# Kernel optimization log

Hardware: AMD Instinct MI355X
Metric: run time of the kernel (lower is better)

The kernel has to match this reference:

```python
import jax, jax.numpy as jnp
import numpy as np

EPS = 1e-5


def setup_inputs() -> dict:
    key = jax.random.key(0)
    k1, k2, k3, k4, k5 = jax.random.split(key, 5)
    B, C, F, O = 32, 64, 16384, 128
    x = jax.random.normal(k1, (B, C, F), dtype=jnp.float32)
    adj = jax.random.randint(k2, (B, F, 4), 0, F, dtype=jnp.int64)
    # Conv1d(C, O, kernel_size=2, stride=2): weight [O, C, 2], bias [O]
    W = jax.random.normal(k3, (O, C, 2), dtype=jnp.float32) * (1.0 / np.sqrt(2 * C))
    b = jax.random.normal(k4, (O,), dtype=jnp.float32) * 0.01
    gamma = jnp.ones((O,), dtype=jnp.float32)
    beta_bn = jnp.zeros((O,), dtype=jnp.float32)
    return {"x": x, "adj": adj, "W": W, "b": b, "gamma": gamma, "beta_bn": beta_bn}


def reference(x, adj, W, b, gamma, beta_bn):
    B, C, F = x.shape
    xt = jnp.transpose(x, (0, 2, 1))                      # [B, F, C]
    # per-batch neighbor gather: re[b, f, k, :] = xt[b, adj[b, f, k], :]
    re = xt[jnp.arange(B)[:, None, None], adj]            # [B, F, 4, C]
    target = re[:, :, 0]                                  # [B, F, C] (alpha)
    neighbors = re[:, :, 1:]                              # [B, F, 3, C]
    beta_f = jnp.sum(jnp.abs(target[:, :, None, :] - neighbors), axis=2)  # [B, F, C]
    # Conv1d(k=2, s=2) over interleaved (alpha, beta) pairs == two matmuls
    y = (jnp.einsum("bfc,oc->bof", target, W[:, :, 0])
         + jnp.einsum("bfc,oc->bof", beta_f, W[:, :, 1])
         + b[None, :, None])                              # [B, O, F]
    # BatchNorm1d (training-mode batch stats over batch and length dims)
    mean = jnp.mean(y, axis=(0, 2), keepdims=True)
    var = jnp.var(y, axis=(0, 2), keepdims=True)
    y = (y - mean) * jax.lax.rsqrt(var + EPS)
    y = y * gamma[None, :, None] + beta_bn[None, :, None]
    return jax.nn.relu(y)
```

## Files before the change

kernel.cpp:

```cpp
#include <hip/hip_runtime.h>

#define B_DIM 32
#define C_DIM 64
#define F_DIM 16384
#define O_DIM 128
#define NBLK ((F_DIM / 64) * B_DIM)

typedef __attribute__((ext_vector_type(8))) short short8;
typedef __attribute__((ext_vector_type(4))) float f32x4;

__device__ __forceinline__ ushort f2bf(float f) {
    union { float f; uint u; } v; v.f = f;
    return (ushort)((v.u + 0x7FFFu + ((v.u >> 16) & 1u)) >> 16);
}
__device__ __forceinline__ float bflo(uint u) {
    union { uint u; float f; } v; v.u = u << 16; return v.f;
}
__device__ __forceinline__ float bfhi(uint u) {
    union { uint u; float f; } v; v.u = u & 0xFFFF0000u; return v.f;
}

__global__ __launch_bounds__(256) void k_transpose(const float* __restrict__ x,
                                                   ushort* __restrict__ xt,
                                                   const float* __restrict__ W,
                                                   ushort* __restrict__ Wtg) {
    __shared__ float tile[64][65];
    const int b  = blockIdx.y;
    const int f0 = blockIdx.x * 64;
    const int t  = threadIdx.x;
    const int fl = t & 63;
    const int q  = t >> 6;

    const float* xb = x + (size_t)b * C_DIM * F_DIM;
    #pragma unroll
    for (int i = 0; i < 16; ++i) {
        const int c = q + i * 4;
        tile[c][fl] = __builtin_nontemporal_load(&xb[(size_t)c * F_DIM + f0 + fl]);
    }

    if (blockIdx.x == 0 && blockIdx.y == 0 && t < 128) {
        const int o = t;
        #pragma unroll 8
        for (int c = 0; c < C_DIM; ++c) {
            Wtg[o * 128 + c]      = f2bf(W[o * 128 + c * 2]);
            Wtg[o * 128 + 64 + c] = f2bf(W[o * 128 + c * 2 + 1]);
        }
    }

    __syncthreads();

    const int f  = t >> 2;
    const int ch = t & 3;
    union { ushort s[16]; uint4 v[2]; } u;
    #pragma unroll
    for (int j = 0; j < 16; ++j)
        u.s[j] = f2bf(tile[ch * 16 + j][f]);
    ushort* dst = xt + ((size_t)b * F_DIM + f0 + f) * C_DIM + ch * 16;
    *(uint4*)(dst)     = u.v[0];
    *(uint4*)(dst + 8) = u.v[1];
}

template <int MODE>
__global__ __launch_bounds__(256, 3) void k_compute_t(const ushort* __restrict__ xt,
                                                      const int*    __restrict__ adj,
                                                      const ushort* __restrict__ Wtg,
                                                      const float*  __restrict__ bias,
                                                      const float*  __restrict__ ss,
                                                      float*        __restrict__ y,
                                                      float*        __restrict__ part) {
    __shared__ __align__(16) char Asm[64 * 256];
    __shared__ __align__(16) char Wsm[128 * 256];

    const int bid = blockIdx.x;
    const int tg  = (bid & 7) * (NBLK / 8) + (bid >> 3);
    const int b   = tg >> 8;
    const int f0  = (tg & 255) * 64;
    const int t   = threadIdx.x;

    const int p  = t >> 2;
    const int ch = t & 3;
    const int4 a4 = ((const int4*)adj)[(size_t)b * F_DIM + f0 + p];
    const char* xb = (const char*)(xt + (size_t)b * F_DIM * C_DIM);
    const char* r0 = xb + (size_t)a4.x * 128 + ch * 32;
    const char* r1 = xb + (size_t)a4.y * 128 + ch * 32;
    const char* r2 = xb + (size_t)a4.z * 128 + ch * 32;
    const char* r3 = xb + (size_t)a4.w * 128 + ch * 32;
    uint4 g[8];
    g[0] = *(const uint4*)(r0);  g[1] = *(const uint4*)(r0 + 16);
    g[2] = *(const uint4*)(r1);  g[3] = *(const uint4*)(r1 + 16);
    g[4] = *(const uint4*)(r2);  g[5] = *(const uint4*)(r2 + 16);
    g[6] = *(const uint4*)(r3);  g[7] = *(const uint4*)(r3 + 16);

    {
        const uint4* src = (const uint4*)Wtg;
        #pragma unroll
        for (int jj = 0; jj < 8; ++jj) {
            const int fb    = t * 128 + jj * 16;
            const int o     = fb >> 8;
            const int inner = fb & 255;
            *(uint4*)(Wsm + (o << 8) + (inner ^ ((o & 7) << 4))) = src[fb >> 4];
        }
    }

    {
        const int sw = (p & 7) << 4;
        char* Arow = Asm + p * 256;
        #pragma unroll
        for (int h = 0; h < 2; ++h) {
            const uint4 t0 = g[h], n1 = g[2 + h], n2 = g[4 + h], n3 = g[6 + h];
            *(uint4*)(Arow + ((ch * 32 + h * 16) ^ sw)) = t0;
            const uint tu[4] = { t0.x, t0.y, t0.z, t0.w };
            const uint au[4] = { n1.x, n1.y, n1.z, n1.w };
            const uint bu[4] = { n2.x, n2.y, n2.z, n2.w };
            const uint cu[4] = { n3.x, n3.y, n3.z, n3.w };
            uint bt[4];
            #pragma unroll
            for (int qq = 0; qq < 4; ++qq) {
                const float tl = bflo(tu[qq]), th = bfhi(tu[qq]);
                const float lo = fabsf(tl - bflo(au[qq])) + fabsf(tl - bflo(bu[qq])) + fabsf(tl - bflo(cu[qq]));
                const float hi = fabsf(th - bfhi(au[qq])) + fabsf(th - bfhi(bu[qq])) + fabsf(th - bfhi(cu[qq]));
                bt[qq] = (uint)f2bf(lo) | ((uint)f2bf(hi) << 16);
            }
            *(uint4*)(Arow + ((128 + ch * 32 + h * 16) ^ sw)) =
                make_uint4(bt[0], bt[1], bt[2], bt[3]);
        }
    }

    __syncthreads();

    const int w     = t >> 6;
    const int l     = t & 63;
    const int col16 = l & 15;
    const int gg    = l >> 4;
    const int swl   = (l & 7) << 4;

    f32x4 acc[8];
    #pragma unroll
    for (int s = 0; s < 8; ++s) {
        const float bv = bias[s * 16 + col16];
        acc[s] = (f32x4){ bv, bv, bv, bv };
    }

    const char* ArowR = Asm + (w * 16 + col16) * 256;
    #pragma unroll
    for (int kk = 0; kk < 4; ++kk) {
        const int koff = kk * 64 + gg * 16;
        const short8 af = *(const short8*)(ArowR + (koff ^ swl));
        #pragma unroll
        for (int s = 0; s < 8; ++s) {
            const short8 bf = *(const short8*)(Wsm + (s * 16 + col16) * 256 + (koff ^ swl));
            acc[s] = __builtin_amdgcn_mfma_f32_16x16x32_bf16(af, bf, acc[s], 0, 0, 0);
        }
    }

    if (MODE == 0) {
        __shared__ float sm_s[4][128];
        __shared__ float sm_q[4][128];
        #pragma unroll
        for (int s = 0; s < 8; ++s) {
            float ps = acc[s].x + acc[s].y + acc[s].z + acc[s].w;
            float pq = acc[s].x * acc[s].x + acc[s].y * acc[s].y
                     + acc[s].z * acc[s].z + acc[s].w * acc[s].w;
            ps += __shfl_xor(ps, 16, 64);  pq += __shfl_xor(pq, 16, 64);
            ps += __shfl_xor(ps, 32, 64);  pq += __shfl_xor(pq, 32, 64);
            if (gg == 0) {
                sm_s[w][s * 16 + col16] = ps;
                sm_q[w][s * 16 + col16] = pq;
            }
        }
        __syncthreads();
        if (t < 128) {
            const float a = sm_s[0][t] + sm_s[1][t] + sm_s[2][t] + sm_s[3][t];
            const float c = sm_q[0][t] + sm_q[1][t] + sm_q[2][t] + sm_q[3][t];
            part[(size_t)t * NBLK + bid]         = a;
            part[(size_t)(128 + t) * NBLK + bid] = c;
        }
    } else {
        const int fbase = f0 + w * 16 + gg * 4;
        #pragma unroll
        for (int s = 0; s < 8; ++s) {
            const int o = s * 16 + col16;
            const float sc = ss[o];
            const float sh = ss[O_DIM + o];
            f32x4 v = acc[s];
            v.x = fmaxf(fmaf(v.x, sc, sh), 0.f);
            v.y = fmaxf(fmaf(v.y, sc, sh), 0.f);
            v.z = fmaxf(fmaf(v.z, sc, sh), 0.f);
            v.w = fmaxf(fmaf(v.w, sc, sh), 0.f);
            __builtin_nontemporal_store(v, (f32x4*)(y + ((size_t)b * O_DIM + o) * F_DIM + fbase));
        }
    }
}

__global__ __launch_bounds__(256) void k_reduce_finalize(const float* __restrict__ part,
                                                         const float* __restrict__ gamma,
                                                         const float* __restrict__ beta_bn,
                                                         float* __restrict__ ss) {
    const int o = blockIdx.x;
    const int t = threadIdx.x;
    const float4* p1 = (const float4*)(part + (size_t)o * NBLK);
    const float4* p2 = (const float4*)(part + (size_t)(128 + o) * NBLK);
    float s = 0.f, q = 0.f;
    for (int i = t; i < NBLK / 4; i += 256) {
        const float4 v = p1[i];
        s += v.x + v.y + v.z + v.w;
        const float4 u = p2[i];
        q += u.x + u.y + u.z + u.w;
    }
    #pragma unroll
    for (int off = 32; off > 0; off >>= 1) {
        s += __shfl_down(s, off, 64);
        q += __shfl_down(q, off, 64);
    }
    __shared__ float ls[8];
    const int wid = t >> 6, lane = t & 63;
    if (lane == 0) { ls[wid] = s; ls[4 + wid] = q; }
    __syncthreads();
    if (t == 0) {
        const float ts = ls[0] + ls[1] + ls[2] + ls[3];
        const float tq = ls[4] + ls[5] + ls[6] + ls[7];
        const float n    = (float)B_DIM * (float)F_DIM;
        const float mean = ts / n;
        const float var  = tq / n - mean * mean;
        const float sc   = gamma[o] * rsqrtf(var + 1e-5f);
        ss[o]         = sc;
        ss[O_DIM + o] = beta_bn[o] - mean * sc;
    }
}

__global__ __launch_bounds__(256) void k_compute_slow(const float* __restrict__ xsrc,
                                                      const int*   __restrict__ adj,
                                                      const float* __restrict__ W,
                                                      const float* __restrict__ bias,
                                                      float*       __restrict__ y) {
    const int b = blockIdx.y;
    const int f = blockIdx.x * 256 + threadIdx.x;
    const int4 a = ((const int4*)adj)[(size_t)b * F_DIM + f];
    float tg[64], bt[64];
    const float* base = xsrc + (size_t)b * C_DIM * F_DIM;
    #pragma unroll
    for (int c = 0; c < 64; ++c) {
        const float tv = base[(size_t)c * F_DIM + a.x];
        const float n1 = base[(size_t)c * F_DIM + a.y];
        const float n2 = base[(size_t)c * F_DIM + a.z];
        const float n3 = base[(size_t)c * F_DIM + a.w];
        tg[c] = tv;
        bt[c] = fabsf(tv - n1) + fabsf(tv - n2) + fabsf(tv - n3);
    }
    float* yb = y + (size_t)b * O_DIM * F_DIM + f;
    const float2* W2 = (const float2*)W;
    #pragma unroll 4
    for (int o = 0; o < O_DIM; ++o) {
        float acc = bias[o];
        #pragma unroll
        for (int c = 0; c < 64; ++c) {
            const float2 wv = W2[o * 64 + c];
            acc = fmaf(tg[c], wv.x, fmaf(bt[c], wv.y, acc));
        }
        yb[(size_t)o * F_DIM] = acc;
    }
}

__global__ __launch_bounds__(256) void k_stats(const float* __restrict__ y,
                                               float* __restrict__ stats) {
    const int o = blockIdx.x;
    const int b = blockIdx.y;
    const float4* row = (const float4*)(y + ((size_t)b * O_DIM + o) * F_DIM);
    float s = 0.f, s2 = 0.f;
    for (int i = threadIdx.x; i < F_DIM / 4; i += 256) {
        const float4 v = row[i];
        s  += v.x + v.y + v.z + v.w;
        s2 += v.x * v.x + v.y * v.y + v.z * v.z + v.w * v.w;
    }
    #pragma unroll
    for (int off = 32; off > 0; off >>= 1) {
        s  += __shfl_down(s,  off, 64);
        s2 += __shfl_down(s2, off, 64);
    }
    __shared__ float ls[4], ls2[4];
    const int wid = threadIdx.x >> 6, lane = threadIdx.x & 63;
    if (lane == 0) { ls[wid] = s; ls2[wid] = s2; }
    __syncthreads();
    if (threadIdx.x == 0) {
        atomicAdd(&stats[o],         ls[0] + ls[1] + ls[2] + ls[3]);
        atomicAdd(&stats[O_DIM + o], ls2[0] + ls2[1] + ls2[2] + ls2[3]);
    }
}

__global__ void k_finalize(const float* __restrict__ stats,
                           const float* __restrict__ gamma,
                           const float* __restrict__ beta_bn,
                           float* __restrict__ ss) {
    const int o = threadIdx.x;
    if (o < O_DIM) {
        const float n    = (float)B_DIM * (float)F_DIM;
        const float mean = stats[o] / n;
        const float var  = stats[O_DIM + o] / n - mean * mean;
        const float sc   = gamma[o] * rsqrtf(var + 1e-5f);
        ss[o]         = sc;
        ss[O_DIM + o] = beta_bn[o] - mean * sc;
    }
}

__global__ __launch_bounds__(256) void k_norm(float* __restrict__ y,
                                              const float* __restrict__ ss) {
    const size_t n4 = (size_t)B_DIM * O_DIM * F_DIM / 4;
    const size_t stride = (size_t)gridDim.x * blockDim.x;
    float4* y4 = (float4*)y;
    for (size_t i = (size_t)blockIdx.x * blockDim.x + threadIdx.x; i < n4; i += stride) {
        const int o = (int)((i >> 12) & (O_DIM - 1));
        const float sc = ss[o];
        const float sh = ss[O_DIM + o];
        float4 v = y4[i];
        v.x = fmaxf(fmaf(v.x, sc, sh), 0.f);
        v.y = fmaxf(fmaf(v.y, sc, sh), 0.f);
        v.z = fmaxf(fmaf(v.z, sc, sh), 0.f);
        v.w = fmaxf(fmaf(v.w, sc, sh), 0.f);
        y4[i] = v;
    }
}

extern "C" void kernel_launch(void* const* d_in, const int* in_sizes, int n_in,
                              void* d_out, int out_size, void* d_ws, size_t ws_size,
                              hipStream_t stream) {
    const float* x       = (const float*)d_in[0];
    const int*   adj     = (const int*)  d_in[1];
    const float* W       = (const float*)d_in[2];
    const float* bias    = (const float*)d_in[3];
    const float* gamma   = (const float*)d_in[4];
    const float* beta_bn = (const float*)d_in[5];
    float* out = (float*)d_out;

    const size_t XT_B   = (size_t)B_DIM * F_DIM * C_DIM * 2;
    const size_t PART_B = (size_t)2 * O_DIM * NBLK * sizeof(float);

    float*  stats = (float*)d_ws;
    float*  ss    = (float*)((char*)d_ws + 1024);
    ushort* Wtg   = (ushort*)((char*)d_ws + 4096);
    ushort* xt    = (ushort*)((char*)d_ws + 65536);
    float*  part  = (float*)((char*)d_ws + 65536 + XT_B);

    const size_t need = 65536 + XT_B + PART_B;

    if (ws_size >= need) {
        k_transpose<<<dim3(F_DIM / 64, B_DIM), 256, 0, stream>>>(x, xt, W, Wtg);
        k_compute_t<0><<<dim3(NBLK), 256, 0, stream>>>(xt, adj, Wtg, bias, nullptr, nullptr, part);
        k_reduce_finalize<<<O_DIM, 256, 0, stream>>>(part, gamma, beta_bn, ss);
        k_compute_t<1><<<dim3(NBLK), 256, 0, stream>>>(xt, adj, Wtg, bias, ss, out, nullptr);
    } else {
        hipMemsetAsync(stats, 0, 2 * O_DIM * sizeof(float), stream);
        k_compute_slow<<<dim3(F_DIM / 256, B_DIM), 256, 0, stream>>>(x, adj, W, bias, out);
        k_stats<<<dim3(O_DIM, B_DIM), 256, 0, stream>>>(out, stats);
        k_finalize<<<1, 128, 0, stream>>>(stats, gamma, beta_bn, ss);
        k_norm<<<2048, 256, 0, stream>>>(out, ss);
    }
}
```

Baseline: 196.5 us.

## Build MFMA A-fragments directly in registers, dropping the LDS A staging tile

Each lane now gathers exactly the channels it needs for its MFMA A-operand fragments and computes the beta (abs-diff sum) values in registers. This removes the 16KB shared A tile, its swizzled writes and reads, and it reorders the K loop so each output slice runs four MFMAs back to back. The smaller LDS footprint lets the launch bound rise to 4 blocks per CU. In exchange, the gathers use 16B accesses at 64B stride per row instead of contiguous 32B chunks, and register pressure may rise under the tighter occupancy bound.

```diff
diff --git a/kernel.cpp b/kernel.cpp
--- a/kernel.cpp
+++ b/kernel.cpp
@@ -18,6 +18,15 @@
 }
 __device__ __forceinline__ float bfhi(uint u) {
     union { uint u; float f; } v; v.u = u & 0xFFFF0000u; return v.f;
+}
+__device__ __forceinline__ uint beta_pair(uint tu, uint au, uint bu, uint cu) {
+    const float tl = bflo(tu), th = bfhi(tu);
+    const float lo = fabsf(tl - bflo(au)) + fabsf(tl - bflo(bu)) + fabsf(tl - bflo(cu));
+    const float hi = fabsf(th - bfhi(au)) + fabsf(th - bfhi(bu)) + fabsf(th - bfhi(cu));
+    return (uint)f2bf(lo) | ((uint)f2bf(hi) << 16);
+}
+__device__ __forceinline__ short8 as_s8(uint4 u) {
+    union { uint4 u; short8 s; } cv; cv.u = u; return cv.s;
 }
 
 __global__ __launch_bounds__(256) void k_transpose(const float* __restrict__ x,
@@ -61,14 +70,13 @@
 }
 
 template <int MODE>
-__global__ __launch_bounds__(256, 3) void k_compute_t(const ushort* __restrict__ xt,
+__global__ __launch_bounds__(256, 4) void k_compute_t(const ushort* __restrict__ xt,
                                                       const int*    __restrict__ adj,
                                                       const ushort* __restrict__ Wtg,
                                                       const float*  __restrict__ bias,
                                                       const float*  __restrict__ ss,
                                                       float*        __restrict__ y,
                                                       float*        __restrict__ part) {
-    __shared__ __align__(16) char Asm[64 * 256];
     __shared__ __align__(16) char Wsm[128 * 256];
 
     const int bid = blockIdx.x;
@@ -77,19 +85,27 @@
     const int f0  = (tg & 255) * 64;
     const int t   = threadIdx.x;
 
-    const int p  = t >> 2;
-    const int ch = t & 3;
+    const int w     = t >> 6;
+    const int l     = t & 63;
+    const int col16 = l & 15;
+    const int g     = l >> 4;
+    const int co    = g * 16;
+    const int p     = w * 16 + col16;
+
     const int4 a4 = ((const int4*)adj)[(size_t)b * F_DIM + f0 + p];
     const char* xb = (const char*)(xt + (size_t)b * F_DIM * C_DIM);
-    const char* r0 = xb + (size_t)a4.x * 128 + ch * 32;
-    const char* r1 = xb + (size_t)a4.y * 128 + ch * 32;
-    const char* r2 = xb + (size_t)a4.z * 128 + ch * 32;
-    const char* r3 = xb + (size_t)a4.w * 128 + ch * 32;
-    uint4 g[8];
-    g[0] = *(const uint4*)(r0);  g[1] = *(const uint4*)(r0 + 16);
-    g[2] = *(const uint4*)(r1);  g[3] = *(const uint4*)(r1 + 16);
-    g[4] = *(const uint4*)(r2);  g[5] = *(const uint4*)(r2 + 16);
-    g[6] = *(const uint4*)(r3);  g[7] = *(const uint4*)(r3 + 16);
+    const char* r0 = xb + (size_t)a4.x * 128 + co;
+    const char* r1 = xb + (size_t)a4.y * 128 + co;
+    const char* r2 = xb + (size_t)a4.z * 128 + co;
+    const char* r3 = xb + (size_t)a4.w * 128 + co;
+    uint4 g0 = *(const uint4*)(r0);
+    uint4 g1 = *(const uint4*)(r0 + 64);
+    uint4 g2 = *(const uint4*)(r1);
+    uint4 g3 = *(const uint4*)(r1 + 64);
+    uint4 g4 = *(const uint4*)(r2);
+    uint4 g5 = *(const uint4*)(r2 + 64);
+    uint4 g6 = *(const uint4*)(r3);
+    uint4 g7 = *(const uint4*)(r3 + 64);
 
     {
         const uint4* src = (const uint4*)Wtg;
@@ -101,38 +117,18 @@
             *(uint4*)(Wsm + (o << 8) + (inner ^ ((o & 7) << 4))) = src[fb >> 4];
         }
     }
-
-    {
-        const int sw = (p & 7) << 4;
-        char* Arow = Asm + p * 256;
-        #pragma unroll
-        for (int h = 0; h < 2; ++h) {
-            const uint4 t0 = g[h], n1 = g[2 + h], n2 = g[4 + h], n3 = g[6 + h];
-            *(uint4*)(Arow + ((ch * 32 + h * 16) ^ sw)) = t0;
-            const uint tu[4] = { t0.x, t0.y, t0.z, t0.w };
-            const uint au[4] = { n1.x, n1.y, n1.z, n1.w };
-            const uint bu[4] = { n2.x, n2.y, n2.z, n2.w };
-            const uint cu[4] = { n3.x, n3.y, n3.z, n3.w };
-            uint bt[4];
-            #pragma unroll
-            for (int qq = 0; qq < 4; ++qq) {
-                const float tl = bflo(tu[qq]), th = bfhi(tu[qq]);
-                const float lo = fabsf(tl - bflo(au[qq])) + fabsf(tl - bflo(bu[qq])) + fabsf(tl - bflo(cu[qq]));
-                const float hi = fabsf(th - bfhi(au[qq])) + fabsf(th - bfhi(bu[qq])) + fabsf(th - bfhi(cu[qq]));
-                bt[qq] = (uint)f2bf(lo) | ((uint)f2bf(hi) << 16);
-            }
-            *(uint4*)(Arow + ((128 + ch * 32 + h * 16) ^ sw)) =
-                make_uint4(bt[0], bt[1], bt[2], bt[3]);
-        }
-    }
-
     __syncthreads();
 
-    const int w     = t >> 6;
-    const int l     = t & 63;
-    const int col16 = l & 15;
-    const int gg    = l >> 4;
-    const int swl   = (l & 7) << 4;
+    short8 af0 = as_s8(g0);
+    short8 af1 = as_s8(g1);
+    short8 af2 = as_s8(make_uint4(beta_pair(g0.x, g2.x, g4.x, g6.x),
+                                  beta_pair(g0.y, g2.y, g4.y, g6.y),
+                                  beta_pair(g0.z, g2.z, g4.z, g6.z),
+                                  beta_pair(g0.w, g2.w, g4.w, g6.w)));
+    short8 af3 = as_s8(make_uint4(beta_pair(g1.x, g3.x, g5.x, g7.x),
+                                  beta_pair(g1.y, g3.y, g5.y, g7.y),
+                                  beta_pair(g1.z, g3.z, g5.z, g7.z),
+                                  beta_pair(g1.w, g3.w, g5.w, g7.w)));
 
     f32x4 acc[8];
     #pragma unroll
@@ -141,16 +137,18 @@
         acc[s] = (f32x4){ bv, bv, bv, bv };
     }
 
-    const char* ArowR = Asm + (w * 16 + col16) * 256;
-    #pragma unroll
-    for (int kk = 0; kk < 4; ++kk) {
-        const int koff = kk * 64 + gg * 16;
-        const short8 af = *(const short8*)(ArowR + (koff ^ swl));
-        #pragma unroll
-        for (int s = 0; s < 8; ++s) {
-            const short8 bf = *(const short8*)(Wsm + (s * 16 + col16) * 256 + (koff ^ swl));
-            acc[s] = __builtin_amdgcn_mfma_f32_16x16x32_bf16(af, bf, acc[s], 0, 0, 0);
-        }
+    const int swl = (col16 & 7) << 4;
+    #pragma unroll
+    for (int s = 0; s < 8; ++s) {
+        const char* Wrow = Wsm + (s * 16 + col16) * 256;
+        acc[s] = __builtin_amdgcn_mfma_f32_16x16x32_bf16(
+                     af0, *(const short8*)(Wrow + ((0 * 64 + g * 16) ^ swl)), acc[s], 0, 0, 0);
+        acc[s] = __builtin_amdgcn_mfma_f32_16x16x32_bf16(
+                     af1, *(const short8*)(Wrow + ((1 * 64 + g * 16) ^ swl)), acc[s], 0, 0, 0);
+        acc[s] = __builtin_amdgcn_mfma_f32_16x16x32_bf16(
+                     af2, *(const short8*)(Wrow + ((2 * 64 + g * 16) ^ swl)), acc[s], 0, 0, 0);
+        acc[s] = __builtin_amdgcn_mfma_f32_16x16x32_bf16(
+                     af3, *(const short8*)(Wrow + ((3 * 64 + g * 16) ^ swl)), acc[s], 0, 0, 0);
     }
 
     if (MODE == 0) {
@@ -163,7 +161,7 @@
                      + acc[s].z * acc[s].z + acc[s].w * acc[s].w;
             ps += __shfl_xor(ps, 16, 64);  pq += __shfl_xor(pq, 16, 64);
             ps += __shfl_xor(ps, 32, 64);  pq += __shfl_xor(pq, 32, 64);
-            if (gg == 0) {
+            if (g == 0) {
                 sm_s[w][s * 16 + col16] = ps;
                 sm_q[w][s * 16 + col16] = pq;
             }
@@ -176,7 +174,7 @@
             part[(size_t)(128 + t) * NBLK + bid] = c;
         }
     } else {
-        const int fbase = f0 + w * 16 + gg * 4;
+        const int fbase = f0 + w * 16 + g * 4;
         #pragma unroll
         for (int s = 0; s < 8; ++s) {
             const int o = s * 16 + col16;
```

Measured after the change: 208.7 us. 6.2% more time.

## Process eight tiles per block with prefetched gathers overlapping MFMA work

Applied to the files above, without the earlier changes.

Each compute block now handles eight consecutive 64-row tiles instead of one. The W tile load into shared memory and the bias/scale reads are amortized across tiles, and the gather loads for the next tile are issued before the MFMA and epilogue of the current one. Per-block statistics accumulate in registers across the tiles, which shrinks the partial-sum buffer and the work of the reduce kernel. The cost is more register pressure, two barriers per tile, and an eighth as many blocks, which lowers parallelism on the grid.

```diff
diff --git a/kernel.cpp b/kernel.cpp
--- a/kernel.cpp
+++ b/kernel.cpp
@@ -4,7 +4,9 @@
 #define C_DIM 64
 #define F_DIM 16384
 #define O_DIM 128
-#define NBLK ((F_DIM / 64) * B_DIM)
+#define NBLK  ((F_DIM / 64) * B_DIM)
+#define TPB   8
+#define NBLK3 (NBLK / TPB)
 
 typedef __attribute__((ext_vector_type(8))) short short8;
 typedef __attribute__((ext_vector_type(4))) float f32x4;
@@ -18,6 +20,12 @@
 }
 __device__ __forceinline__ float bfhi(uint u) {
     union { uint u; float f; } v; v.u = u & 0xFFFF0000u; return v.f;
+}
+__device__ __forceinline__ uint beta_pair(uint tu, uint au, uint bu, uint cu) {
+    const float tl = bflo(tu), th = bfhi(tu);
+    const float lo = fabsf(tl - bflo(au)) + fabsf(tl - bflo(bu)) + fabsf(tl - bflo(cu));
+    const float hi = fabsf(th - bfhi(au)) + fabsf(th - bfhi(bu)) + fabsf(th - bfhi(cu));
+    return (uint)f2bf(lo) | ((uint)f2bf(hi) << 16);
 }
 
 __global__ __launch_bounds__(256) void k_transpose(const float* __restrict__ x,
@@ -71,25 +79,40 @@
     __shared__ __align__(16) char Asm[64 * 256];
     __shared__ __align__(16) char Wsm[128 * 256];
 
-    const int bid = blockIdx.x;
-    const int tg  = (bid & 7) * (NBLK / 8) + (bid >> 3);
-    const int b   = tg >> 8;
-    const int f0  = (tg & 255) * 64;
-    const int t   = threadIdx.x;
+    const int bid  = blockIdx.x;
+    const int tg0  = ((bid & 7) * (NBLK3 / 8) + (bid >> 3)) * TPB;
+    const int b    = tg0 >> 8;
+    const int tloc = tg0 & 255;
+    const int t    = threadIdx.x;
 
     const int p  = t >> 2;
     const int ch = t & 3;
-    const int4 a4 = ((const int4*)adj)[(size_t)b * F_DIM + f0 + p];
-    const char* xb = (const char*)(xt + (size_t)b * F_DIM * C_DIM);
-    const char* r0 = xb + (size_t)a4.x * 128 + ch * 32;
-    const char* r1 = xb + (size_t)a4.y * 128 + ch * 32;
-    const char* r2 = xb + (size_t)a4.z * 128 + ch * 32;
-    const char* r3 = xb + (size_t)a4.w * 128 + ch * 32;
-    uint4 g[8];
-    g[0] = *(const uint4*)(r0);  g[1] = *(const uint4*)(r0 + 16);
-    g[2] = *(const uint4*)(r1);  g[3] = *(const uint4*)(r1 + 16);
-    g[4] = *(const uint4*)(r2);  g[5] = *(const uint4*)(r2 + 16);
-    g[6] = *(const uint4*)(r3);  g[7] = *(const uint4*)(r3 + 16);
+    const int4* adjp = (const int4*)adj + (size_t)b * F_DIM;
+    const char* xb   = (const char*)(xt + (size_t)b * F_DIM * C_DIM);
+
+    const int4 a0 = adjp[(tloc + 0) * 64 + p];
+    const int4 a1 = adjp[(tloc + 1) * 64 + p];
+    const int4 a2 = adjp[(tloc + 2) * 64 + p];
+    const int4 a3 = adjp[(tloc + 3) * 64 + p];
+    const int4 a4_ = adjp[(tloc + 4) * 64 + p];
+    const int4 a5 = adjp[(tloc + 5) * 64 + p];
+    const int4 a6 = adjp[(tloc + 6) * 64 + p];
+    const int4 a7 = adjp[(tloc + 7) * 64 + p];
+
+    uint4 g0, g1, g2, g3, g4, g5, g6, g7;
+    #define ISSUE(a)                                                          \
+        do {                                                                  \
+            g0 = *(const uint4*)(xb + (size_t)(a).x * 128 + ch * 32);         \
+            g1 = *(const uint4*)(xb + (size_t)(a).x * 128 + ch * 32 + 16);    \
+            g2 = *(const uint4*)(xb + (size_t)(a).y * 128 + ch * 32);         \
+            g3 = *(const uint4*)(xb + (size_t)(a).y * 128 + ch * 32 + 16);    \
+            g4 = *(const uint4*)(xb + (size_t)(a).z * 128 + ch * 32);         \
+            g5 = *(const uint4*)(xb + (size_t)(a).z * 128 + ch * 32 + 16);    \
+            g6 = *(const uint4*)(xb + (size_t)(a).w * 128 + ch * 32);         \
+            g7 = *(const uint4*)(xb + (size_t)(a).w * 128 + ch * 32 + 16);    \
+        } while (0)
+
+    ISSUE(a0);
 
     {
         const uint4* src = (const uint4*)Wtg;
@@ -102,92 +125,120 @@
         }
     }
 
-    {
-        const int sw = (p & 7) << 4;
-        char* Arow = Asm + p * 256;
-        #pragma unroll
-        for (int h = 0; h < 2; ++h) {
-            const uint4 t0 = g[h], n1 = g[2 + h], n2 = g[4 + h], n3 = g[6 + h];
-            *(uint4*)(Arow + ((ch * 32 + h * 16) ^ sw)) = t0;
-            const uint tu[4] = { t0.x, t0.y, t0.z, t0.w };
-            const uint au[4] = { n1.x, n1.y, n1.z, n1.w };
-            const uint bu[4] = { n2.x, n2.y, n2.z, n2.w };
-            const uint cu[4] = { n3.x, n3.y, n3.z, n3.w };
-            uint bt[4];
-            #pragma unroll
-            for (int qq = 0; qq < 4; ++qq) {
-                const float tl = bflo(tu[qq]), th = bfhi(tu[qq]);
-                const float lo = fabsf(tl - bflo(au[qq])) + fabsf(tl - bflo(bu[qq])) + fabsf(tl - bflo(cu[qq]));
-                const float hi = fabsf(th - bfhi(au[qq])) + fabsf(th - bfhi(bu[qq])) + fabsf(th - bfhi(cu[qq]));
-                bt[qq] = (uint)f2bf(lo) | ((uint)f2bf(hi) << 16);
-            }
-            *(uint4*)(Arow + ((128 + ch * 32 + h * 16) ^ sw)) =
-                make_uint4(bt[0], bt[1], bt[2], bt[3]);
-        }
-    }
-
-    __syncthreads();
-
     const int w     = t >> 6;
     const int l     = t & 63;
     const int col16 = l & 15;
-    const int gg    = l >> 4;
+    const int kg    = l >> 4;
     const int swl   = (l & 7) << 4;
-
-    f32x4 acc[8];
-    #pragma unroll
-    for (int s = 0; s < 8; ++s) {
-        const float bv = bias[s * 16 + col16];
-        acc[s] = (f32x4){ bv, bv, bv, bv };
-    }
-
+    const int swp   = (p & 7) << 4;
+    char* Arow = Asm + p * 256;
     const char* ArowR = Asm + (w * 16 + col16) * 256;
-    #pragma unroll
-    for (int kk = 0; kk < 4; ++kk) {
-        const int koff = kk * 64 + gg * 16;
-        const short8 af = *(const short8*)(ArowR + (koff ^ swl));
+
+    float bv[8];
+    #pragma unroll
+    for (int s = 0; s < 8; ++s) bv[s] = bias[s * 16 + col16];
+    float scv[8], shv[8];
+    if (MODE == 1) {
         #pragma unroll
         for (int s = 0; s < 8; ++s) {
-            const short8 bf = *(const short8*)(Wsm + (s * 16 + col16) * 256 + (koff ^ swl));
-            acc[s] = __builtin_amdgcn_mfma_f32_16x16x32_bf16(af, bf, acc[s], 0, 0, 0);
-        }
-    }
+            scv[s] = ss[s * 16 + col16];
+            shv[s] = ss[O_DIM + s * 16 + col16];
+        }
+    }
+    float ps[8], pq[8];
+    if (MODE == 0) {
+        #pragma unroll
+        for (int s = 0; s < 8; ++s) { ps[s] = 0.f; pq[s] = 0.f; }
+    }
+
+    #define WRITE_A()                                                              \
+        do {                                                                       \
+            *(uint4*)(Arow + ((ch * 32 + 0)  ^ swp)) = g0;                         \
+            *(uint4*)(Arow + ((ch * 32 + 16) ^ swp)) = g1;                         \
+            *(uint4*)(Arow + ((128 + ch * 32 + 0) ^ swp)) =                        \
+                make_uint4(beta_pair(g0.x, g2.x, g4.x, g6.x),                      \
+                           beta_pair(g0.y, g2.y, g4.y, g6.y),                      \
+                           beta_pair(g0.z, g2.z, g4.z, g6.z),                      \
+                           beta_pair(g0.w, g2.w, g4.w, g6.w));                     \
+            *(uint4*)(Arow + ((128 + ch * 32 + 16) ^ swp)) =                       \
+                make_uint4(beta_pair(g1.x, g3.x, g5.x, g7.x),                      \
+                           beta_pair(g1.y, g3.y, g5.y, g7.y),                      \
+                           beta_pair(g1.z, g3.z, g5.z, g7.z),                      \
+                           beta_pair(g1.w, g3.w, g5.w, g7.w));                     \
+        } while (0)
+
+    #define MFMA_EPI(i)                                                            \
+        do {                                                                       \
+            f32x4 acc[8];                                                          \
+            _Pragma("unroll")                                                      \
+            for (int s = 0; s < 8; ++s) acc[s] = (f32x4){bv[s], bv[s], bv[s], bv[s]}; \
+            _Pragma("unroll")                                                      \
+            for (int kk = 0; kk < 4; ++kk) {                                       \
+                const int koff = kk * 64 + kg * 16;                                \
+                const short8 af = *(const short8*)(ArowR + (koff ^ swl));          \
+                _Pragma("unroll")                                                  \
+                for (int s = 0; s < 8; ++s) {                                      \
+                    const short8 bf = *(const short8*)(Wsm + (s * 16 + col16) * 256 \
+                                                        + (koff ^ swl));           \
+                    acc[s] = __builtin_amdgcn_mfma_f32_16x16x32_bf16(af, bf, acc[s], 0, 0, 0); \
+                }                                                                  \
+            }                                                                      \
+            if (MODE == 0) {                                                       \
+                _Pragma("unroll")                                                  \
+                for (int s = 0; s < 8; ++s) {                                      \
+                    ps[s] += acc[s].x + acc[s].y + acc[s].z + acc[s].w;            \
+                    pq[s] += acc[s].x * acc[s].x + acc[s].y * acc[s].y             \
+                           + acc[s].z * acc[s].z + acc[s].w * acc[s].w;            \
+                }                                                                  \
+            } else {                                                               \
+                const int fbase = (tloc + (i)) * 64 + w * 16 + kg * 4;             \
+                _Pragma("unroll")                                                  \
+                for (int s = 0; s < 8; ++s) {                                      \
+                    const int o = s * 16 + col16;                                  \
+                    f32x4 v = acc[s];                                              \
+                    v.x = fmaxf(fmaf(v.x, scv[s], shv[s]), 0.f);                   \
+                    v.y = fmaxf(fmaf(v.y, scv[s], shv[s]), 0.f);                   \
+                    v.z = fmaxf(fmaf(v.z, scv[s], shv[s]), 0.f);                   \
+                    v.w = fmaxf(fmaf(v.w, scv[s], shv[s]), 0.f);                   \
+                    __builtin_nontemporal_store(v,                                  \
+                        (f32x4*)(y + ((size_t)b * O_DIM + o) * F_DIM + fbase));    \
+                }                                                                  \
+            }                                                                      \
+        } while (0)
+
+    WRITE_A();  __syncthreads();  ISSUE(a1);  MFMA_EPI(0);  __syncthreads();
+    WRITE_A();  __syncthreads();  ISSUE(a2);  MFMA_EPI(1);  __syncthreads();
+    WRITE_A();  __syncthreads();  ISSUE(a3);  MFMA_EPI(2);  __syncthreads();
+    WRITE_A();  __syncthreads();  ISSUE(a4_); MFMA_EPI(3);  __syncthreads();
+    WRITE_A();  __syncthreads();  ISSUE(a5);  MFMA_EPI(4);  __syncthreads();
+    WRITE_A();  __syncthreads();  ISSUE(a6);  MFMA_EPI(5);  __syncthreads();
+    WRITE_A();  __syncthreads();  ISSUE(a7);  MFMA_EPI(6);  __syncthreads();
+    WRITE_A();  __syncthreads();              MFMA_EPI(7);
+
+    #undef ISSUE
+    #undef WRITE_A
+    #undef MFMA_EPI
 
     if (MODE == 0) {
         __shared__ float sm_s[4][128];
         __shared__ float sm_q[4][128];
+        __syncthreads();
         #pragma unroll
         for (int s = 0; s < 8; ++s) {
-            float ps = acc[s].x + acc[s].y + acc[s].z + acc[s].w;
-            float pq = acc[s].x * acc[s].x + acc[s].y * acc[s].y
-                     + acc[s].z * acc[s].z + acc[s].w * acc[s].w;
-            ps += __shfl_xor(ps, 16, 64);  pq += __shfl_xor(pq, 16, 64);
-            ps += __shfl_xor(ps, 32, 64);  pq += __shfl_xor(pq, 32, 64);
-            if (gg == 0) {
-                sm_s[w][s * 16 + col16] = ps;
-                sm_q[w][s * 16 + col16] = pq;
+            float a = ps[s], c = pq[s];
+            a += __shfl_xor(a, 16, 64);  c += __shfl_xor(c, 16, 64);
+            a += __shfl_xor(a, 32, 64);  c += __shfl_xor(c, 32, 64);
+            if (kg == 0) {
+                sm_s[w][s * 16 + col16] = a;
+                sm_q[w][s * 16 + col16] = c;
             }
         }
         __syncthreads();
         if (t < 128) {
             const float a = sm_s[0][t] + sm_s[1][t] + sm_s[2][t] + sm_s[3][t];
             const float c = sm_q[0][t] + sm_q[1][t] + sm_q[2][t] + sm_q[3][t];
-            part[(size_t)t * NBLK + bid]         = a;
-            part[(size_t)(128 + t) * NBLK + bid] = c;
-        }
-    } else {
-        const int fbase = f0 + w * 16 + gg * 4;
-        #pragma unroll
-        for (int s = 0; s < 8; ++s) {
-            const int o = s * 16 + col16;
-            const float sc = ss[o];
-            const float sh = ss[O_DIM + o];
-            f32x4 v = acc[s];
-            v.x = fmaxf(fmaf(v.x, sc, sh), 0.f);
-            v.y = fmaxf(fmaf(v.y, sc, sh), 0.f);
-            v.z = fmaxf(fmaf(v.z, sc, sh), 0.f);
-            v.w = fmaxf(fmaf(v.w, sc, sh), 0.f);
-            __builtin_nontemporal_store(v, (f32x4*)(y + ((size_t)b * O_DIM + o) * F_DIM + fbase));
+            part[(size_t)t * NBLK3 + bid]         = a;
+            part[(size_t)(128 + t) * NBLK3 + bid] = c;
         }
     }
 }
@@ -198,10 +249,10 @@
                                                          float* __restrict__ ss) {
     const int o = blockIdx.x;
     const int t = threadIdx.x;
-    const float4* p1 = (const float4*)(part + (size_t)o * NBLK);
-    const float4* p2 = (const float4*)(part + (size_t)(128 + o) * NBLK);
+    const float4* p1 = (const float4*)(part + (size_t)o * NBLK3);
+    const float4* p2 = (const float4*)(part + (size_t)(128 + o) * NBLK3);
     float s = 0.f, q = 0.f;
-    for (int i = t; i < NBLK / 4; i += 256) {
+    for (int i = t; i < NBLK3 / 4; i += 256) {
         const float4 v = p1[i];
         s += v.x + v.y + v.z + v.w;
         const float4 u = p2[i];
@@ -332,7 +383,7 @@
     float* out = (float*)d_out;
 
     const size_t XT_B   = (size_t)B_DIM * F_DIM * C_DIM * 2;
-    const size_t PART_B = (size_t)2 * O_DIM * NBLK * sizeof(float);
+    const size_t PART_B = (size_t)2 * O_DIM * NBLK3 * sizeof(float);
 
     float*  stats = (float*)d_ws;
     float*  ss    = (float*)((char*)d_ws + 1024);
@@ -344,9 +395,9 @@
 
     if (ws_size >= need) {
         k_transpose<<<dim3(F_DIM / 64, B_DIM), 256, 0, stream>>>(x, xt, W, Wtg);
-        k_compute_t<0><<<dim3(NBLK), 256, 0, stream>>>(xt, adj, Wtg, bias, nullptr, nullptr, part);
+        k_compute_t<0><<<dim3(NBLK3), 256, 0, stream>>>(xt, adj, Wtg, bias, nullptr, nullptr, part);
         k_reduce_finalize<<<O_DIM, 256, 0, stream>>>(part, gamma, beta_bn, ss);
-        k_compute_t<1><<<dim3(NBLK), 256, 0, stream>>>(xt, adj, Wtg, bias, ss, out, nullptr);
+        k_compute_t<1><<<dim3(NBLK3), 256, 0, stream>>>(xt, adj, Wtg, bias, ss, out, nullptr);
     } else {
         hipMemsetAsync(stats, 0, 2 * O_DIM * sizeof(float), stream);
         k_compute_slow<<<dim3(F_DIM / 256, B_DIM), 256, 0, stream>>>(x, adj, W, bias, out);
```

Measured after the change: 208.6 us. +6.2%, slower.
